# Kernel optimization log

Measured on AMD Instinct MI355X. Metric: run time of the kernel, lower is better.

The kernel has to match this reference:

```python
import jax, jax.numpy as jnp
import numpy as np

THRESHOLDS = (0.3, 0.4, 0.5)
EPS_NORM = 1e-12   # F.normalize eps
EPS_MAX = 1e-5     # added to max before rescale


def setup_inputs() -> dict:
    key = jax.random.key(0)
    k1, k2 = jax.random.split(key)
    cam = jax.random.uniform(k1, (4, 64, 64), dtype=jnp.float32)
    feat = jax.random.normal(k2, (4, 256, 64, 64), dtype=jnp.float32)
    return {"cam": cam, "feat": feat}


def reference(cam, feat):
    # multi-threshold soft mask: mean of hard masks at each threshold -> (B,1,H,W)
    masks = jnp.stack([(cam >= t).astype(feat.dtype) for t in THRESHOLDS], axis=1)
    m = masks.mean(axis=1)[:, None]  # (B,1,H,W)
    masked = feat * m  # (B,C,H,W)

    B, C, H, W = masked.shape
    f = masked.reshape(B, C, H * W)  # (B,C,N)
    # L2-normalize over channel dim (torch F.normalize, dim=1)
    norm = jnp.sqrt(jnp.sum(f * f, axis=1, keepdims=True))
    fn = f / jnp.maximum(norm, EPS_NORM)

    # full pairwise similarity (B,N,N), then CAM-weighted aggregation
    sim = jnp.einsum('bcn,bcm->bnm', fn, fn)      # (B,N,N)
    camf = cam.reshape(B, H * W)                  # (B,N)
    out = jnp.einsum('bnm,bm->bn', sim, camf)     # (B,N)

    mn = out.min(axis=1, keepdims=True)
    mx = out.max(axis=1, keepdims=True) + EPS_MAX
    ref = ((out - mn) / (mx - mn)).reshape(B, H, W)

    loss = jnp.mean(jnp.abs(ref - jax.lax.stop_gradient(cam)))
    return ref, loss
```

## Files before the change

kernel.cpp:

```cpp
#include <hip/hip_runtime.h>


constexpr int B    = 4;
constexpr int C    = 256;
constexpr int N    = 4096;
constexpr int BN   = B * N;
constexpr int CN   = C * N;
constexpr int NBLK = 512;

#define SCOPE_AGENT __HIP_MEMORY_SCOPE_AGENT

__device__ __forceinline__ float wsum(float v) {
#pragma unroll
    for (int o = 32; o > 0; o >>= 1) v += __shfl_down(v, o, 64);
    return v;
}
__device__ __forceinline__ float wmin64(float v) {
#pragma unroll
    for (int o = 32; o > 0; o >>= 1) v = fminf(v, __shfl_down(v, o, 64));
    return v;
}
__device__ __forceinline__ float wmax64(float v) {
#pragma unroll
    for (int o = 32; o > 0; o >>= 1) v = fmaxf(v, __shfl_down(v, o, 64));
    return v;
}

__global__ void __launch_bounds__(256) k_norm_vpart(
    const float* __restrict__ cam, const float* __restrict__ feat,
    float* __restrict__ s, float* __restrict__ v_part,
    unsigned int* __restrict__ cnt)
{
    if (blockIdx.x == 0 && threadIdx.x == 0) *cnt = 0u;

    __shared__ float red4[32][33];
    __shared__ float w_sh[32];

    const int t  = threadIdx.x;
    const int qu = t & 7;
    const int G  = t >> 3;
    const int bk = blockIdx.x;
    const int b  = bk >> 7;
    const int n0 = (bk * 32) & (N - 1);

    const float* fp = feat + (size_t)b * CN + n0 + qu * 4;
    float4 x[8];
    float4 ss = make_float4(0.f, 0.f, 0.f, 0.f);
#pragma unroll
    for (int it = 0; it < 8; ++it) {
        x[it] = *(const float4*)(fp + (size_t)(it * 32 + G) * N);
        ss.x = fmaf(x[it].x, x[it].x, ss.x);
        ss.y = fmaf(x[it].y, x[it].y, ss.y);
        ss.z = fmaf(x[it].z, x[it].z, ss.z);
        ss.w = fmaf(x[it].w, x[it].w, ss.w);
    }
    red4[G][qu * 4 + 0] = ss.x;
    red4[G][qu * 4 + 1] = ss.y;
    red4[G][qu * 4 + 2] = ss.z;
    red4[G][qu * 4 + 3] = ss.w;
    __syncthreads();

    if (t < 32) {
        float tot = 0.f;
#pragma unroll
        for (int g = 0; g < 32; ++g) tot += red4[g][t];
        float cv = cam[bk * 32 + t];
        float m  = ((cv >= 0.3f ? 1.f : 0.f) + (cv >= 0.4f ? 1.f : 0.f) +
                    (cv >= 0.5f ? 1.f : 0.f)) * (1.f / 3.f);
        float sc = m / fmaxf(m * sqrtf(tot), 1e-12f);
        s[bk * 32 + t] = sc;
        w_sh[t] = sc * cv;
    }
    __syncthreads();

    float4 wq = *(const float4*)&w_sh[qu * 4];
    float vp[8];
#pragma unroll
    for (int it = 0; it < 8; ++it) {
        float a = fmaf(x[it].x, wq.x,
                  fmaf(x[it].y, wq.y,
                  fmaf(x[it].z, wq.z, x[it].w * wq.w)));
#pragma unroll
        for (int o = 4; o > 0; o >>= 1) a += __shfl_down(a, o, 8);
        vp[it] = a;
    }
    if (qu == 0) {
#pragma unroll
        for (int it = 0; it < 8; ++it)
            v_part[bk * 256 + it * 32 + G] = vp[it];
    }
}

__global__ void __launch_bounds__(256) k_vreduce(
    const float* __restrict__ v_part, float* __restrict__ v)
{
    __shared__ float vred[4][64];
    const int t  = threadIdx.x;
    const int l  = t & 63;
    const int ks = t >> 6;
    const int bc = blockIdx.x * 64 + l;
    const int vb = bc >> 8, c = bc & 255;
    const float* vp = v_part + (size_t)vb * (128 * 256) + c;
    float a = 0.f;
#pragma unroll
    for (int kk = 0; kk < 32; ++kk)
        a += vp[(size_t)(ks * 32 + kk) * 256];
    vred[ks][l] = a;
    __syncthreads();
    if (t < 64)
        v[bc] = (vred[0][t] + vred[1][t]) + (vred[2][t] + vred[3][t]);
}

__global__ void __launch_bounds__(256) k_out(
    const float* __restrict__ feat, const float* __restrict__ s,
    const float* __restrict__ v, float* __restrict__ ob,
    float* __restrict__ bmn, float* __restrict__ bmx)
{
    __shared__ float vs[C];
    __shared__ float red4[32][33];

    const int t  = threadIdx.x;
    const int qu = t & 7;
    const int G  = t >> 3;
    const int bk = blockIdx.x;
    const int b  = bk >> 7;
    const int n0 = (bk * 32) & (N - 1);

    vs[t] = v[b * C + t];
    __syncthreads();

    const float* fp = feat + (size_t)b * CN + n0 + qu * 4;
    float4 acc = make_float4(0.f, 0.f, 0.f, 0.f);
#pragma unroll
    for (int it = 0; it < 8; ++it) {
        float4 xx = *(const float4*)(fp + (size_t)(it * 32 + G) * N);
        float vc = vs[it * 32 + G];
        acc.x = fmaf(xx.x, vc, acc.x);
        acc.y = fmaf(xx.y, vc, acc.y);
        acc.z = fmaf(xx.z, vc, acc.z);
        acc.w = fmaf(xx.w, vc, acc.w);
    }
    red4[G][qu * 4 + 0] = acc.x;
    red4[G][qu * 4 + 1] = acc.y;
    red4[G][qu * 4 + 2] = acc.z;
    red4[G][qu * 4 + 3] = acc.w;
    __syncthreads();

    if (t < 32) {
        float tot = 0.f;
#pragma unroll
        for (int g = 0; g < 32; ++g) tot += red4[g][t];
        float o = s[bk * 32 + t] * tot;
        ob[bk * 32 + t] = o;
        float mn = o, mx = o;
#pragma unroll
        for (int o2 = 16; o2 > 0; o2 >>= 1) {
            mn = fminf(mn, __shfl_down(mn, o2, 64));
            mx = fmaxf(mx, __shfl_down(mx, o2, 64));
        }
        if (t == 0) { bmn[bk] = mn; bmx[bk] = mx; }
    }
}

__global__ void __launch_bounds__(256) k_final(
    const float* __restrict__ ob, const float* __restrict__ cam,
    const float* __restrict__ bmn, const float* __restrict__ bmx,
    float* __restrict__ out, float* __restrict__ part, unsigned int* __restrict__ cnt)
{
    const int t = threadIdx.x, blk = blockIdx.x;
    const int p = blk * 256 + t;
    const int b = blk >> 4;

    __shared__ float sh[2];
    if (t < 64) {
        float a = fminf(bmn[b * 128 + t], bmn[b * 128 + 64 + t]);
        a = wmin64(a);
        if (t == 0) sh[0] = a;
    } else if (t < 128) {
        int l = t - 64;
        float a = fmaxf(bmx[b * 128 + l], bmx[b * 128 + 64 + l]);
        a = wmax64(a);
        if (l == 0) sh[1] = a;
    }
    __syncthreads();
    const float mn = sh[0];
    const float mx = sh[1] + 1e-5f;

    float r = (ob[p] - mn) / (mx - mn);
    out[p] = r;
    float ad = fabsf(r - cam[p]);

    __shared__ float red[4];
    float ps = wsum(ad);
    if ((t & 63) == 0) red[t >> 6] = ps;
    __syncthreads();

    __shared__ int lastflag;
    if (t == 0) {
        float tot = (red[0] + red[1]) + (red[2] + red[3]);
        __hip_atomic_store(&part[blk], tot, __ATOMIC_RELEASE, SCOPE_AGENT);
        unsigned old = __hip_atomic_fetch_add(cnt, 1u, __ATOMIC_ACQ_REL, SCOPE_AGENT);
        lastflag = (old == 63u) ? 1 : 0;
    }
    __syncthreads();
    if (lastflag && t < 64) {
        float x = __hip_atomic_load(&part[t], __ATOMIC_ACQUIRE, SCOPE_AGENT);
        x = wsum(x);
        if (t == 0) out[BN] = x * (1.f / (float)BN);
    }
}

extern "C" void kernel_launch(void* const* d_in, const int* in_sizes, int n_in,
                              void* d_out, int out_size, void* d_ws, size_t ws_size,
                              hipStream_t stream) {
    const float* cam  = (const float*)d_in[0];
    const float* feat = (const float*)d_in[1];
    float* out = (float*)d_out;
    float* ws  = (float*)d_ws;

    float* s      = ws;
    float* v_part = ws + 16384;
    float* v      = ws + 147456;
    float* ob     = ws + 148480;
    float* bmn    = ws + 164864;
    float* bmx    = ws + 165376;
    float* part   = ws + 165888;
    unsigned int* cnt = (unsigned int*)(ws + 165952);

    k_norm_vpart<<<NBLK, 256, 0, stream>>>(cam, feat, s, v_part, cnt);
    k_vreduce   <<<16,   256, 0, stream>>>(v_part, v);
    k_out       <<<NBLK, 256, 0, stream>>>(feat, s, v, ob, bmn, bmx);
    k_final     <<<64,   256, 0, stream>>>(ob, cam, bmn, bmx, out, part, cnt);
}
```

Measured before the change: 19.00 us.

## Fuse reduction kernels into producers via last-block atomic rank tails

Merges the v-reduce kernel into the front kernel and the final normalize/loss kernel into the output kernel. The last NFIN blocks to arrive, ranked by an atomic counter, spin until all blocks have published their partials and then do the reduction tail. This cuts four launches to two plus a memset and removes two inter-kernel gaps. The cost is spin-waiting, atomic traffic, and reliance on the late-ranked blocks being resident while they wait.

```diff
diff --git a/kernel.cpp b/kernel.cpp
--- a/kernel.cpp
+++ b/kernel.cpp
@@ -7,6 +7,7 @@
 constexpr int BN   = B * N;
 constexpr int CN   = C * N;
 constexpr int NBLK = 512;
+constexpr int NFIN = 16;
 
 #define SCOPE_AGENT __HIP_MEMORY_SCOPE_AGENT
 
@@ -26,15 +27,15 @@
     return v;
 }
 
-__global__ void __launch_bounds__(256) k_norm_vpart(
+__global__ void __launch_bounds__(256) k_front(
     const float* __restrict__ cam, const float* __restrict__ feat,
-    float* __restrict__ s, float* __restrict__ v_part,
+    float* __restrict__ s, float* __restrict__ v_part, float* __restrict__ v,
     unsigned int* __restrict__ cnt)
 {
-    if (blockIdx.x == 0 && threadIdx.x == 0) *cnt = 0u;
-
     __shared__ float red4[32][33];
     __shared__ float w_sh[32];
+    __shared__ float vred[4][64];
+    __shared__ unsigned rank_sh;
 
     const int t  = threadIdx.x;
     const int qu = t & 7;
@@ -87,37 +88,49 @@
     if (qu == 0) {
 #pragma unroll
         for (int it = 0; it < 8; ++it)
-            v_part[bk * 256 + it * 32 + G] = vp[it];
-    }
-}
-
-__global__ void __launch_bounds__(256) k_vreduce(
-    const float* __restrict__ v_part, float* __restrict__ v)
-{
-    __shared__ float vred[4][64];
-    const int t  = threadIdx.x;
+            __hip_atomic_store(&v_part[bk * 256 + it * 32 + G], vp[it],
+                               __ATOMIC_RELAXED, SCOPE_AGENT);
+    }
+    __syncthreads();
+    if (t == 0)
+        rank_sh = __hip_atomic_fetch_add(&cnt[0], 1u, __ATOMIC_ACQ_REL, SCOPE_AGENT);
+    __syncthreads();
+    const unsigned rank = rank_sh;
+    if (rank < (unsigned)(NBLK - NFIN)) return;
+
+    const int slice = (int)rank - (NBLK - NFIN);
+    if (t == 0)
+        while (__hip_atomic_load(&cnt[0], __ATOMIC_ACQUIRE, SCOPE_AGENT) < (unsigned)NBLK)
+            __builtin_amdgcn_s_sleep(1);
+    __syncthreads();
+
     const int l  = t & 63;
     const int ks = t >> 6;
-    const int bc = blockIdx.x * 64 + l;
+    const int bc = slice * 64 + l;
     const int vb = bc >> 8, c = bc & 255;
-    const float* vp = v_part + (size_t)vb * (128 * 256) + c;
     float a = 0.f;
 #pragma unroll
     for (int kk = 0; kk < 32; ++kk)
-        a += vp[(size_t)(ks * 32 + kk) * 256];
+        a += __hip_atomic_load(
+                 &v_part[(size_t)(vb * 128 + ks * 32 + kk) * 256 + c],
+                 __ATOMIC_RELAXED, SCOPE_AGENT);
     vred[ks][l] = a;
     __syncthreads();
     if (t < 64)
         v[bc] = (vred[0][t] + vred[1][t]) + (vred[2][t] + vred[3][t]);
 }
 
-__global__ void __launch_bounds__(256) k_out(
+__global__ void __launch_bounds__(256) k_back(
     const float* __restrict__ feat, const float* __restrict__ s,
-    const float* __restrict__ v, float* __restrict__ ob,
-    float* __restrict__ bmn, float* __restrict__ bmx)
+    const float* __restrict__ v, const float* __restrict__ cam,
+    float* __restrict__ ob, float* __restrict__ bmn, float* __restrict__ bmx,
+    float* __restrict__ part, float* __restrict__ out,
+    unsigned int* __restrict__ cnt)
 {
     __shared__ float vs[C];
     __shared__ float red4[32][33];
+    __shared__ float shmn[4], shmx[4], redl[4];
+    __shared__ unsigned rank_sh;
 
     const int t  = threadIdx.x;
     const int qu = t & 7;
@@ -151,62 +164,71 @@
 #pragma unroll
         for (int g = 0; g < 32; ++g) tot += red4[g][t];
         float o = s[bk * 32 + t] * tot;
-        ob[bk * 32 + t] = o;
+        __hip_atomic_store(&ob[bk * 32 + t], o, __ATOMIC_RELAXED, SCOPE_AGENT);
         float mn = o, mx = o;
 #pragma unroll
         for (int o2 = 16; o2 > 0; o2 >>= 1) {
             mn = fminf(mn, __shfl_down(mn, o2, 64));
             mx = fmaxf(mx, __shfl_down(mx, o2, 64));
         }
-        if (t == 0) { bmn[bk] = mn; bmx[bk] = mx; }
-    }
-}
-
-__global__ void __launch_bounds__(256) k_final(
-    const float* __restrict__ ob, const float* __restrict__ cam,
-    const float* __restrict__ bmn, const float* __restrict__ bmx,
-    float* __restrict__ out, float* __restrict__ part, unsigned int* __restrict__ cnt)
-{
-    const int t = threadIdx.x, blk = blockIdx.x;
-    const int p = blk * 256 + t;
-    const int b = blk >> 4;
-
-    __shared__ float sh[2];
-    if (t < 64) {
-        float a = fminf(bmn[b * 128 + t], bmn[b * 128 + 64 + t]);
+        if (t == 0) {
+            __hip_atomic_store(&bmn[bk], mn, __ATOMIC_RELAXED, SCOPE_AGENT);
+            __hip_atomic_store(&bmx[bk], mx, __ATOMIC_RELAXED, SCOPE_AGENT);
+        }
+    }
+    __syncthreads();
+    if (t == 0)
+        rank_sh = __hip_atomic_fetch_add(&cnt[1], 1u, __ATOMIC_ACQ_REL, SCOPE_AGENT);
+    __syncthreads();
+    const unsigned rank = rank_sh;
+    if (rank < (unsigned)(NBLK - NFIN)) return;
+
+    const int slice = (int)rank - (NBLK - NFIN);
+    if (t == 0)
+        while (__hip_atomic_load(&cnt[1], __ATOMIC_ACQUIRE, SCOPE_AGENT) < (unsigned)NBLK)
+            __builtin_amdgcn_s_sleep(1);
+    __syncthreads();
+
+    const int w = t >> 6, l = t & 63;
+    {
+        float a = fminf(
+            __hip_atomic_load(&bmn[w * 128 + l],      __ATOMIC_RELAXED, SCOPE_AGENT),
+            __hip_atomic_load(&bmn[w * 128 + 64 + l], __ATOMIC_RELAXED, SCOPE_AGENT));
         a = wmin64(a);
-        if (t == 0) sh[0] = a;
-    } else if (t < 128) {
-        int l = t - 64;
-        float a = fmaxf(bmx[b * 128 + l], bmx[b * 128 + 64 + l]);
-        a = wmax64(a);
-        if (l == 0) sh[1] = a;
-    }
-    __syncthreads();
-    const float mn = sh[0];
-    const float mx = sh[1] + 1e-5f;
-
-    float r = (ob[p] - mn) / (mx - mn);
-    out[p] = r;
-    float ad = fabsf(r - cam[p]);
-
-    __shared__ float red[4];
-    float ps = wsum(ad);
-    if ((t & 63) == 0) red[t >> 6] = ps;
-    __syncthreads();
-
-    __shared__ int lastflag;
+        float z = fmaxf(
+            __hip_atomic_load(&bmx[w * 128 + l],      __ATOMIC_RELAXED, SCOPE_AGENT),
+            __hip_atomic_load(&bmx[w * 128 + 64 + l], __ATOMIC_RELAXED, SCOPE_AGENT));
+        z = wmax64(z);
+        if (l == 0) { shmn[w] = a; shmx[w] = z; }
+    }
+    __syncthreads();
+
+    const int bb = slice >> 2;
+    const float mn  = shmn[bb];
+    const float mxa = shmx[bb] + 1e-5f;
+    float lsum = 0.f;
+#pragma unroll
+    for (int i = 0; i < 4; ++i) {
+        int p = slice * 1024 + i * 256 + t;
+        float o = __hip_atomic_load(&ob[p], __ATOMIC_RELAXED, SCOPE_AGENT);
+        float r = (o - mn) / (mxa - mn);
+        out[p] = r;
+        lsum += fabsf(r - cam[p]);
+    }
+    float ps = wsum(lsum);
+    if (l == 0) redl[w] = ps;
+    __syncthreads();
     if (t == 0) {
-        float tot = (red[0] + red[1]) + (red[2] + red[3]);
-        __hip_atomic_store(&part[blk], tot, __ATOMIC_RELEASE, SCOPE_AGENT);
-        unsigned old = __hip_atomic_fetch_add(cnt, 1u, __ATOMIC_ACQ_REL, SCOPE_AGENT);
-        lastflag = (old == 63u) ? 1 : 0;
-    }
-    __syncthreads();
-    if (lastflag && t < 64) {
-        float x = __hip_atomic_load(&part[t], __ATOMIC_ACQUIRE, SCOPE_AGENT);
-        x = wsum(x);
-        if (t == 0) out[BN] = x * (1.f / (float)BN);
+        float tot = (redl[0] + redl[1]) + (redl[2] + redl[3]);
+        __hip_atomic_store(&part[slice], tot, __ATOMIC_RELEASE, SCOPE_AGENT);
+        unsigned o2 = __hip_atomic_fetch_add(&cnt[2], 1u, __ATOMIC_ACQ_REL, SCOPE_AGENT);
+        if (o2 == (unsigned)(NFIN - 1)) {
+            float x = 0.f;
+#pragma unroll
+            for (int j = 0; j < NFIN; ++j)
+                x += __hip_atomic_load(&part[j], __ATOMIC_RELAXED, SCOPE_AGENT);
+            out[BN] = x * (1.f / (float)BN);
+        }
     }
 }
 
@@ -227,8 +249,7 @@
     float* part   = ws + 165888;
     unsigned int* cnt = (unsigned int*)(ws + 165952);
 
-    k_norm_vpart<<<NBLK, 256, 0, stream>>>(cam, feat, s, v_part, cnt);
-    k_vreduce   <<<16,   256, 0, stream>>>(v_part, v);
-    k_out       <<<NBLK, 256, 0, stream>>>(feat, s, v, ob, bmn, bmx);
-    k_final     <<<64,   256, 0, stream>>>(ob, cam, bmn, bmx, out, part, cnt);
-}
+    hipMemsetAsync((void*)cnt, 0, 3 * sizeof(unsigned int), stream);
+    k_front<<<NBLK, 256, 0, stream>>>(cam, feat, s, v_part, v, cnt);
+    k_back <<<NBLK, 256, 0, stream>>>(feat, s, v, cam, ob, bmn, bmx, part, out, cnt);
+}
```

Measured after the change: 39.74 us. 2.09x slower.
